# Optimization experiments

Measured on AMD Instinct MI355X. Metric: run time of the kernel, lower is better.

The kernel has to match this reference:

```python
import jax, jax.numpy as jnp
import numpy as np

EPS = 1e-5
D_MODEL, D_INNER, D_STATE, DT_RANK, K = 2048, 4096, 16, 128, 4

def setup_inputs() -> dict:
    key = jax.random.key(0)
    ks = jax.random.split(key, 13)
    B = 128
    s = lambda k, shape, sc=0.02: jax.random.normal(k, shape, jnp.float32) * sc
    return {
        "hidden_states": jax.random.normal(ks[0], (B, 1, D_MODEL), jnp.float32),
        "conv_state": jax.random.normal(ks[1], (B, D_INNER, K - 1), jnp.float32),
        "ssm_state": jax.random.normal(ks[2], (B, D_INNER, D_STATE), jnp.float32),
        "norm_w": jnp.ones((D_MODEL,), jnp.float32),
        "in_proj_w": s(ks[3], (2 * D_INNER, D_MODEL)),           # no bias (HF Mamba default)
        "conv_w": s(ks[4], (D_INNER, K), 0.1),                    # depthwise conv kernel
        "conv_b": s(ks[5], (D_INNER,), 0.1),
        "x_proj_w": s(ks[6], (DT_RANK + 2 * D_STATE, D_INNER)),
        "dt_proj_w": s(ks[7], (D_INNER, DT_RANK)),
        "dt_proj_b": s(ks[8], (D_INNER,), 0.1),
        "A_log": jnp.log(jnp.broadcast_to(jnp.arange(1, D_STATE + 1, dtype=jnp.float32), (D_INNER, D_STATE))),
        "D": jnp.ones((D_INNER,), jnp.float32),
        "out_proj_w": s(ks[9], (D_MODEL, D_INNER)),               # no bias
    }

def reference(hidden_states, conv_state, ssm_state, norm_w, in_proj_w, conv_w, conv_b,
              x_proj_w, dt_proj_w, dt_proj_b, A_log, D, out_proj_w):
    x = hidden_states[:, 0, :]                                   # (B, d_model)
    # RMSNorm (pre-norm)
    normed = x * jax.lax.rsqrt(jnp.mean(x * x, axis=-1, keepdims=True) + EPS) * norm_w
    # in_proj -> gate z and conv branch xc
    xz = normed @ in_proj_w.T                                    # (B, 2*d_inner)
    xc, z = jnp.split(xz, 2, axis=-1)
    # depthwise causal conv, single-step with rolling cache
    conv_in = jnp.concatenate([conv_state, xc[:, :, None]], axis=-1)  # (B, d_inner, K)
    new_conv_state = conv_in[:, :, 1:]
    xact = jax.nn.silu(jnp.sum(conv_in * conv_w[None], axis=-1) + conv_b)  # (B, d_inner)
    # input-dependent SSM params
    proj = xact @ x_proj_w.T                                     # (B, dt_rank + 2*d_state)
    dt_raw = proj[:, :DT_RANK]
    Bmat = proj[:, DT_RANK:DT_RANK + D_STATE]                    # (B, d_state)
    Cmat = proj[:, DT_RANK + D_STATE:]                           # (B, d_state)
    dt = jax.nn.softplus(dt_raw @ dt_proj_w.T + dt_proj_b)       # (B, d_inner)
    A = -jnp.exp(A_log)                                          # (d_inner, d_state)
    dA = jnp.exp(dt[:, :, None] * A[None])                       # (B, d_inner, d_state)
    dB = dt[:, :, None] * Bmat[:, None, :]
    new_ssm_state = ssm_state * dA + dB * xact[:, :, None]
    y = jnp.sum(new_ssm_state * Cmat[:, None, :], axis=-1) + D * xact
    y = y * jax.nn.silu(z)
    out = y @ out_proj_w.T                                       # (B, d_model)
    output = out[:, None, :] + hidden_states                     # residual add
    return output, new_conv_state, new_ssm_state
```

## Files before the change

kernel.cpp:

```cpp
#include <hip/hip_runtime.h>

typedef __attribute__((ext_vector_type(8))) short bf16x8;
typedef __attribute__((ext_vector_type(4))) float f32x4;
typedef __attribute__((ext_vector_type(8))) unsigned short u16x8;
typedef __attribute__((ext_vector_type(4))) unsigned short u16x4;

#define DM 2048
#define DI 4096
#define BATCH 128

__device__ __forceinline__ unsigned short f2bf(float f) {
  union { float f; unsigned u; } v; v.f = f;
  unsigned r = v.u + 0x7FFFu + ((v.u >> 16) & 1u);
  return (unsigned short)(r >> 16);
}
__device__ __forceinline__ float bf2f(unsigned short u) {
  union { unsigned u; float f; } v; v.u = (unsigned)u << 16; return v.f;
}
__device__ __forceinline__ float sigm(float x) { return 1.f / (1.f + __expf(-x)); }

constexpr int BK = 64;
constexpr int LDT = BK + 8;

#define LDREGS(AR, ARF, BR, kb_) do {                                                     \
    int kb = (kb_);                                                                       \
    if constexpr (ABF) {                                                                  \
      _Pragma("unroll") for (int i = 0; i < 4; ++i) {                                     \
        int idx = tid + i * 256, r = idx >> 3, c = (idx & 7) * 8;                         \
        AR[i] = *(const u16x8*)&((const unsigned short*)Ag)[(long)r * lda + kb + c];      \
      }                                                                                   \
    } else {                                                                              \
      _Pragma("unroll") for (int i = 0; i < 8; ++i) {                                     \
        int idx = tid + i * 256, r = idx >> 4, c = (idx & 15) * 4;                        \
        ARF[i] = *(const f32x4*)&((const float*)Ag)[(long)r * lda + kb + c];              \
      }                                                                                   \
    }                                                                                     \
    _Pragma("unroll") for (int i = 0; i < BN / 16; ++i) {                                 \
      int idx = tid + i * 256, r = idx >> 4, c = (idx & 15) * 4;                          \
      BR[i] = *(const f32x4*)&Bg[(long)(n0 + r) * ldb + kb + c];                          \
    }                                                                                     \
  } while (0)

#define STLDS(AR, ARF, BR, buf_) do {                                                     \
    unsigned short* As_ = lds + (buf_) * BUF;                                             \
    unsigned short* Bs_ = As_ + 128 * LDT;                                                \
    if constexpr (ABF) {                                                                  \
      _Pragma("unroll") for (int i = 0; i < 4; ++i) {                                     \
        int idx = tid + i * 256, r = idx >> 3, c = (idx & 7) * 8;                         \
        *(u16x8*)&As_[r * LDT + c] = AR[i];                                               \
      }                                                                                   \
    } else {                                                                              \
      _Pragma("unroll") for (int i = 0; i < 8; ++i) {                                     \
        int idx = tid + i * 256, r = idx >> 4, c = (idx & 15) * 4;                        \
        u16x4 o; o[0] = f2bf(ARF[i][0]); o[1] = f2bf(ARF[i][1]);                          \
        o[2] = f2bf(ARF[i][2]); o[3] = f2bf(ARF[i][3]);                                   \
        *(u16x4*)&As_[r * LDT + c] = o;                                                   \
      }                                                                                   \
    }                                                                                     \
    _Pragma("unroll") for (int i = 0; i < BN / 16; ++i) {                                 \
      int idx = tid + i * 256, r = idx >> 4, c = (idx & 15) * 4;                          \
      u16x4 o; o[0] = f2bf(BR[i][0]); o[1] = f2bf(BR[i][1]);                              \
      o[2] = f2bf(BR[i][2]); o[3] = f2bf(BR[i][3]);                                       \
      *(u16x4*)&Bs_[r * LDT + c] = o;                                                     \
    }                                                                                     \
  } while (0)

#define COMPUTE(buf_) do {                                                                \
    const unsigned short* As_ = lds + (buf_) * BUF;                                       \
    const unsigned short* Bs_ = As_ + 128 * LDT;                                          \
    _Pragma("unroll") for (int kk = 0; kk < BK; kk += 32) {                               \
      int kr = kk + lhi * 8;                                                              \
      bf16x8 af[4], bfr[NF];                                                              \
      _Pragma("unroll") for (int mi = 0; mi < 4; ++mi)                                    \
        af[mi] = *(const bf16x8*)&As_[(wm * 64 + mi * 16 + llo) * LDT + kr];              \
      _Pragma("unroll") for (int ni = 0; ni < NF; ++ni)                                   \
        bfr[ni] = *(const bf16x8*)&Bs_[(wn * 16 * NF + ni * 16 + llo) * LDT + kr];        \
      _Pragma("unroll") for (int mi = 0; mi < 4; ++mi)                                    \
        _Pragma("unroll") for (int ni = 0; ni < NF; ++ni)                                 \
          acc[mi * NF + ni] = __builtin_amdgcn_mfma_f32_16x16x32_bf16(                    \
              af[mi], bfr[ni], acc[mi * NF + ni], 0, 0, 0);                               \
    }                                                                                     \
  } while (0)

template<int BN, bool ABF>
__device__ __forceinline__ void gemm128(const void* Ag, int lda, const float* Bg, int ldb,
                                        int n0, int k0, int k1, unsigned short* lds,
                                        f32x4* acc) {
  constexpr int NF = BN / 32;
  constexpr int BUF = (128 + BN) * LDT;
  const int tid = threadIdx.x, lane = tid & 63, wave = tid >> 6;
  const int wm = wave >> 1, wn = wave & 1, llo = lane & 15, lhi = lane >> 4;

  u16x8 ar0[ABF ? 4 : 1], ar1[ABF ? 4 : 1];
  f32x4 arf0[ABF ? 1 : 8], arf1[ABF ? 1 : 8];
  f32x4 br0[BN / 16], br1[BN / 16];

  const int nt = (k1 - k0) / BK;
  LDREGS(ar0, arf0, br0, k0);
  LDREGS(ar1, arf1, br1, k0 + BK);
  STLDS(ar0, arf0, br0, 0);
  __syncthreads();
  int t = 0;
  while (true) {
    if (t + 2 < nt) LDREGS(ar0, arf0, br0, k0 + (t + 2) * BK);
    COMPUTE(0);
    if (t + 1 < nt) STLDS(ar1, arf1, br1, 1);
    __syncthreads();
    if (++t == nt) break;
    if (t + 2 < nt) LDREGS(ar1, arf1, br1, k0 + (t + 2) * BK);
    COMPUTE(1);
    if (t + 1 < nt) STLDS(ar0, arf0, br0, 0);
    __syncthreads();
    if (++t == nt) break;
  }
}

__global__ __launch_bounds__(256) void k01_prep(const float* __restrict__ hs,
                                                const float* __restrict__ nw,
                                                unsigned short* __restrict__ normed,
                                                float* __restrict__ outp,
                                                float* __restrict__ xz,
                                                float* __restrict__ proj) {
  int blk = blockIdx.x, tid = threadIdx.x;
  int t = blk * 256 + tid;
  f32x4 z = {};
  *(f32x4*)&xz[t * 4] = z;
  if (t < 65536) *(f32x4*)&outp[t * 4] = *(const f32x4*)&hs[t * 4];
  if (t < 5120) *(f32x4*)&proj[t * 4] = z;
  if (blk < 128) {
    int b = blk;
    const float* xr = hs + (long)b * DM;
    f32x4 v0 = *(const f32x4*)&xr[tid * 4];
    f32x4 v1 = *(const f32x4*)&xr[(tid + 256) * 4];
    float ss = v0[0]*v0[0] + v0[1]*v0[1] + v0[2]*v0[2] + v0[3]*v0[3]
             + v1[0]*v1[0] + v1[1]*v1[1] + v1[2]*v1[2] + v1[3]*v1[3];
    for (int off = 32; off; off >>= 1) ss += __shfl_xor(ss, off);
    __shared__ float red[4];
    if ((tid & 63) == 0) red[tid >> 6] = ss;
    __syncthreads();
    ss = red[0] + red[1] + red[2] + red[3];
    float rstd = rsqrtf(ss * (1.f / DM) + 1e-5f);
    f32x4 w0 = *(const f32x4*)&nw[tid * 4];
    f32x4 w1 = *(const f32x4*)&nw[(tid + 256) * 4];
    u16x4 o0, o1;
#pragma unroll
    for (int j = 0; j < 4; ++j) {
      o0[j] = f2bf(v0[j] * rstd * w0[j]);
      o1[j] = f2bf(v1[j] * rstd * w1[j]);
    }
    *(u16x4*)&normed[(long)b * DM + tid * 4] = o0;
    *(u16x4*)&normed[(long)b * DM + (tid + 256) * 4] = o1;
  }
}

__global__ __launch_bounds__(256) void k2_inproj(const unsigned short* __restrict__ normed,
                                                 const float* __restrict__ W,
                                                 float* __restrict__ xz) {
  __shared__ unsigned short lds[2 * (128 + 64) * LDT];
  f32x4 acc[8] = {};
  int bn = blockIdx.x, sk = blockIdx.y;
  gemm128<64, true>(normed, DM, W, DM, bn * 64, sk * 512, sk * 512 + 512, lds, acc);
  int tid = threadIdx.x, lane = tid & 63, wave = tid >> 6, wm = wave >> 1, wn = wave & 1;
  int llo = lane & 15, lhi = lane >> 4;
#pragma unroll
  for (int mi = 0; mi < 4; ++mi)
#pragma unroll
    for (int ni = 0; ni < 2; ++ni)
#pragma unroll
      for (int r = 0; r < 4; ++r) {
        int b = wm * 64 + mi * 16 + lhi * 4 + r;
        int n = bn * 64 + wn * 32 + ni * 16 + llo;
        atomicAdd(&xz[(long)b * 8192 + n], acc[mi * 2 + ni][r]);
      }
}

__global__ __launch_bounds__(256) void e2_conv(const float* __restrict__ xz,
                                               const float* __restrict__ conv_state,
                                               const float* __restrict__ conv_w,
                                               const float* __restrict__ conv_b,
                                               float* __restrict__ out_ncs,
                                               float* __restrict__ xact_f,
                                               unsigned short* __restrict__ xact_b,
                                               unsigned short* __restrict__ szb) {
  int p = blockIdx.x * 256 + threadIdx.x;
  int b = p >> 12, n = p & 4095;
  float xc = xz[(long)b * 8192 + n];
  float z  = xz[(long)b * 8192 + DI + n];
  const float* cs = conv_state + (long)p * 3;
  float c0 = cs[0], c1 = cs[1], c2 = cs[2];
  f32x4 cw = *(const f32x4*)&conv_w[n * 4];
  float xs = c0 * cw[0] + c1 * cw[1] + c2 * cw[2] + xc * cw[3] + conv_b[n];
  float xa = xs * sigm(xs);
  float* ncs = out_ncs + (long)p * 3;
  ncs[0] = c1; ncs[1] = c2; ncs[2] = xc;
  xact_f[p] = xa;
  xact_b[p] = f2bf(xa);
  szb[p] = f2bf(z * sigm(z));
}

__global__ __launch_bounds__(256) void k3_xproj(const unsigned short* __restrict__ xact_b,
                                                const float* __restrict__ XW,
                                                float* __restrict__ proj) {
  __shared__ unsigned short lds[2 * (128 + 32) * LDT];
  f32x4 acc[4] = {};
  int bn = blockIdx.x, kc = blockIdx.y;
  gemm128<32, true>(xact_b, DI, XW, DI, bn * 32, kc * 128, kc * 128 + 128, lds, acc);
  int tid = threadIdx.x, lane = tid & 63, wave = tid >> 6, wm = wave >> 1, wn = wave & 1;
  int llo = lane & 15, lhi = lane >> 4;
  int n = bn * 32 + wn * 16 + llo;
#pragma unroll
  for (int mi = 0; mi < 4; ++mi)
#pragma unroll
    for (int r = 0; r < 4; ++r) {
      int b = wm * 64 + mi * 16 + lhi * 4 + r;
      atomicAdd(&proj[b * 160 + n], acc[mi][r]);
    }
}

__global__ __launch_bounds__(256) void k4a_dt(const float* __restrict__ proj,
                                              const float* __restrict__ DW,
                                              const float* __restrict__ dtb,
                                              float* __restrict__ dt_f) {
  __shared__ unsigned short lds[2 * (128 + 32) * LDT];
  f32x4 acc[4] = {};
  int bn = blockIdx.x;
  gemm128<32, false>(proj, 160, DW, 128, bn * 32, 0, 128, lds, acc);
  int tid = threadIdx.x, lane = tid & 63, wave = tid >> 6, wm = wave >> 1, wn = wave & 1;
  int llo = lane & 15, lhi = lane >> 4;
  int n = bn * 32 + wn * 16 + llo;
  float db = dtb[n];
#pragma unroll
  for (int mi = 0; mi < 4; ++mi)
#pragma unroll
    for (int r = 0; r < 4; ++r) {
      int b = wm * 64 + mi * 16 + lhi * 4 + r;
      float v = acc[mi][r] + db;
      dt_f[(long)b * DI + n] = (v > 20.f) ? v : log1pf(__expf(v));
    }
}

__global__ __launch_bounds__(256) void k4b_ssm(const float* __restrict__ dt_f,
                                               const float* __restrict__ proj,
                                               const float* __restrict__ A_log,
                                               const float* __restrict__ Dp,
                                               const float* __restrict__ ssm,
                                               const float* __restrict__ xact_f,
                                               const unsigned short* __restrict__ szb,
                                               float* __restrict__ out_nss,
                                               unsigned short* __restrict__ yz_b) {
  int t = blockIdx.x * 256 + threadIdx.x;
  int s4 = t & 3;
  int p0 = t >> 2;
  const int STRIDE = (2048 * 256) >> 2;
#pragma unroll
  for (int it = 0; it < 4; ++it) {
    int p = p0 + it * STRIDE;
    int b = p >> 12, n = p & 4095;
    float dtv = dt_f[p];
    float xa = xact_f[p];
    f32x4 sv = *(const f32x4*)&ssm[(long)p * 16 + s4 * 4];
    f32x4 Al = *(const f32x4*)&A_log[n * 16 + s4 * 4];
    f32x4 Bv = *(const f32x4*)&proj[b * 160 + 128 + s4 * 4];
    f32x4 Cv = *(const f32x4*)&proj[b * 160 + 144 + s4 * 4];
    f32x4 nv;
    float y = 0.f;
#pragma unroll
    for (int j = 0; j < 4; ++j) {
      float dA = __expf(dtv * (-__expf(Al[j])));
      nv[j] = sv[j] * dA + dtv * Bv[j] * xa;
      y += nv[j] * Cv[j];
    }
    *(f32x4*)&out_nss[(long)p * 16 + s4 * 4] = nv;
    y += __shfl_xor(y, 1);
    y += __shfl_xor(y, 2);
    if (s4 == 0) yz_b[p] = f2bf((y + Dp[n] * xa) * bf2f(szb[p]));
  }
}

__global__ __launch_bounds__(256) void k5_outproj(const unsigned short* __restrict__ yz_b,
                                                  const float* __restrict__ OW,
                                                  float* __restrict__ outp) {
  __shared__ unsigned short lds[2 * (128 + 32) * LDT];
  f32x4 acc[4] = {};
  int bn = blockIdx.x, sk = blockIdx.y;
  gemm128<32, true>(yz_b, DI, OW, DI, bn * 32, sk * 512, sk * 512 + 512, lds, acc);
  int tid = threadIdx.x, lane = tid & 63, wave = tid >> 6, wm = wave >> 1, wn = wave & 1;
  int llo = lane & 15, lhi = lane >> 4;
  int n = bn * 32 + wn * 16 + llo;
#pragma unroll
  for (int mi = 0; mi < 4; ++mi)
#pragma unroll
    for (int r = 0; r < 4; ++r) {
      int b = wm * 64 + mi * 16 + lhi * 4 + r;
      atomicAdd(&outp[(long)b * DM + n], acc[mi][r]);
    }
}

extern "C" void kernel_launch(void* const* d_in, const int* in_sizes, int n_in, void* d_out,
                              int out_size, void* d_ws, size_t ws_size, hipStream_t stream) {
  const float* hs         = (const float*)d_in[0];
  const float* conv_state = (const float*)d_in[1];
  const float* ssm        = (const float*)d_in[2];
  const float* norm_w     = (const float*)d_in[3];
  const float* in_proj_w  = (const float*)d_in[4];
  const float* conv_w     = (const float*)d_in[5];
  const float* conv_b     = (const float*)d_in[6];
  const float* x_proj_w   = (const float*)d_in[7];
  const float* dt_proj_w  = (const float*)d_in[8];
  const float* dt_proj_b  = (const float*)d_in[9];
  const float* A_log      = (const float*)d_in[10];
  const float* Dp         = (const float*)d_in[11];
  const float* out_proj_w = (const float*)d_in[12];

  float* outp    = (float*)d_out;
  float* out_ncs = outp + 262144;
  float* out_nss = outp + 262144 + 1572864;

  char* ws = (char*)d_ws;
  unsigned short* normed = (unsigned short*)(ws);
  float*          dt_f   = (float*)(ws);
  float*          xz     = (float*)(ws + 2097152);
  unsigned short* yz_b   = (unsigned short*)(ws + 2097152);
  float*          xact_f = (float*)(ws + 6291456);
  unsigned short* xact_b = (unsigned short*)(ws + 8388608);
  unsigned short* szb    = (unsigned short*)(ws + 9437184);
  float*          proj   = (float*)(ws + 10485760);

  hipLaunchKernelGGL(k01_prep, dim3(1024), dim3(256), 0, stream, hs, norm_w, normed, outp, xz, proj);
  hipLaunchKernelGGL(k2_inproj, dim3(128, 4), dim3(256), 0, stream, normed, in_proj_w, xz);
  hipLaunchKernelGGL(e2_conv, dim3(2048), dim3(256), 0, stream, xz, conv_state, conv_w, conv_b,
                     out_ncs, xact_f, xact_b, szb);
  hipLaunchKernelGGL(k3_xproj, dim3(5, 32), dim3(256), 0, stream, xact_b, x_proj_w, proj);
  hipLaunchKernelGGL(k4a_dt, dim3(128), dim3(256), 0, stream, proj, dt_proj_w, dt_proj_b, dt_f);
  hipLaunchKernelGGL(k4b_ssm, dim3(2048), dim3(256), 0, stream, dt_f, proj, A_log, Dp, ssm,
                     xact_f, szb, out_nss, yz_b);
  hipLaunchKernelGGL(k5_outproj, dim3(64, 8), dim3(256), 0, stream, yz_b, out_proj_w, outp);
}
```

Measured before the change: 76.76 us.

## Fuse dt projection GEMM with SSM update and shrink in_proj N tile

Generalizes the GEMM helper to take an M tile size and offset. It then fuses the dt_proj GEMM and softplus into the selective-scan update kernel, so the dt intermediate is never written to or read from global memory and one launch disappears. The fused kernel uses 32x32 tiles over a 128x4 grid, and each thread handles all 16 states of a row with per-thread strided 64-byte loads. The in_proj kernel also switches from a 64-wide to a 32-wide N tile, doubling its block count for better occupancy. That costs more reloading of the A operand.

```diff
diff --git a/kernel.cpp b/kernel.cpp
--- a/kernel.cpp
+++ b/kernel.cpp
@@ -25,14 +25,14 @@
 #define LDREGS(AR, ARF, BR, kb_) do {                                                     \
     int kb = (kb_);                                                                       \
     if constexpr (ABF) {                                                                  \
-      _Pragma("unroll") for (int i = 0; i < 4; ++i) {                                     \
+      _Pragma("unroll") for (int i = 0; i < BM / 32; ++i) {                               \
         int idx = tid + i * 256, r = idx >> 3, c = (idx & 7) * 8;                         \
-        AR[i] = *(const u16x8*)&((const unsigned short*)Ag)[(long)r * lda + kb + c];      \
+        AR[i] = *(const u16x8*)&((const unsigned short*)Ag)[(long)(m0 + r) * lda + kb + c]; \
       }                                                                                   \
     } else {                                                                              \
-      _Pragma("unroll") for (int i = 0; i < 8; ++i) {                                     \
+      _Pragma("unroll") for (int i = 0; i < BM / 16; ++i) {                               \
         int idx = tid + i * 256, r = idx >> 4, c = (idx & 15) * 4;                        \
-        ARF[i] = *(const f32x4*)&((const float*)Ag)[(long)r * lda + kb + c];              \
+        ARF[i] = *(const f32x4*)&((const float*)Ag)[(long)(m0 + r) * lda + kb + c];       \
       }                                                                                   \
     }                                                                                     \
     _Pragma("unroll") for (int i = 0; i < BN / 16; ++i) {                                 \
@@ -43,14 +43,14 @@
 
 #define STLDS(AR, ARF, BR, buf_) do {                                                     \
     unsigned short* As_ = lds + (buf_) * BUF;                                             \
-    unsigned short* Bs_ = As_ + 128 * LDT;                                                \
+    unsigned short* Bs_ = As_ + BM * LDT;                                                 \
     if constexpr (ABF) {                                                                  \
-      _Pragma("unroll") for (int i = 0; i < 4; ++i) {                                     \
+      _Pragma("unroll") for (int i = 0; i < BM / 32; ++i) {                               \
         int idx = tid + i * 256, r = idx >> 3, c = (idx & 7) * 8;                         \
         *(u16x8*)&As_[r * LDT + c] = AR[i];                                               \
       }                                                                                   \
     } else {                                                                              \
-      _Pragma("unroll") for (int i = 0; i < 8; ++i) {                                     \
+      _Pragma("unroll") for (int i = 0; i < BM / 16; ++i) {                               \
         int idx = tid + i * 256, r = idx >> 4, c = (idx & 15) * 4;                        \
         u16x4 o; o[0] = f2bf(ARF[i][0]); o[1] = f2bf(ARF[i][1]);                          \
         o[2] = f2bf(ARF[i][2]); o[3] = f2bf(ARF[i][3]);                                   \
@@ -67,32 +67,33 @@
 
 #define COMPUTE(buf_) do {                                                                \
     const unsigned short* As_ = lds + (buf_) * BUF;                                       \
-    const unsigned short* Bs_ = As_ + 128 * LDT;                                          \
+    const unsigned short* Bs_ = As_ + BM * LDT;                                           \
     _Pragma("unroll") for (int kk = 0; kk < BK; kk += 32) {                               \
       int kr = kk + lhi * 8;                                                              \
-      bf16x8 af[4], bfr[NF];                                                              \
-      _Pragma("unroll") for (int mi = 0; mi < 4; ++mi)                                    \
-        af[mi] = *(const bf16x8*)&As_[(wm * 64 + mi * 16 + llo) * LDT + kr];              \
+      bf16x8 af[MI], bfr[NF];                                                             \
+      _Pragma("unroll") for (int mi = 0; mi < MI; ++mi)                                   \
+        af[mi] = *(const bf16x8*)&As_[(wm * (BM / 2) + mi * 16 + llo) * LDT + kr];        \
       _Pragma("unroll") for (int ni = 0; ni < NF; ++ni)                                   \
         bfr[ni] = *(const bf16x8*)&Bs_[(wn * 16 * NF + ni * 16 + llo) * LDT + kr];        \
-      _Pragma("unroll") for (int mi = 0; mi < 4; ++mi)                                    \
+      _Pragma("unroll") for (int mi = 0; mi < MI; ++mi)                                   \
         _Pragma("unroll") for (int ni = 0; ni < NF; ++ni)                                 \
           acc[mi * NF + ni] = __builtin_amdgcn_mfma_f32_16x16x32_bf16(                    \
               af[mi], bfr[ni], acc[mi * NF + ni], 0, 0, 0);                               \
     }                                                                                     \
   } while (0)
 
-template<int BN, bool ABF>
-__device__ __forceinline__ void gemm128(const void* Ag, int lda, const float* Bg, int ldb,
-                                        int n0, int k0, int k1, unsigned short* lds,
-                                        f32x4* acc) {
+template<int BM, int BN, bool ABF>
+__device__ __forceinline__ void gemmMN(const void* Ag, int lda, const float* Bg, int ldb,
+                                       int m0, int n0, int k0, int k1, unsigned short* lds,
+                                       f32x4* acc) {
   constexpr int NF = BN / 32;
-  constexpr int BUF = (128 + BN) * LDT;
+  constexpr int MI = BM / 32;
+  constexpr int BUF = (BM + BN) * LDT;
   const int tid = threadIdx.x, lane = tid & 63, wave = tid >> 6;
   const int wm = wave >> 1, wn = wave & 1, llo = lane & 15, lhi = lane >> 4;
 
-  u16x8 ar0[ABF ? 4 : 1], ar1[ABF ? 4 : 1];
-  f32x4 arf0[ABF ? 1 : 8], arf1[ABF ? 1 : 8];
+  u16x8 ar0[ABF ? BM / 32 : 1], ar1[ABF ? BM / 32 : 1];
+  f32x4 arf0[ABF ? 1 : BM / 16], arf1[ABF ? 1 : BM / 16];
   f32x4 br0[BN / 16], br1[BN / 16];
 
   const int nt = (k1 - k0) / BK;
@@ -156,22 +157,20 @@
 __global__ __launch_bounds__(256) void k2_inproj(const unsigned short* __restrict__ normed,
                                                  const float* __restrict__ W,
                                                  float* __restrict__ xz) {
-  __shared__ unsigned short lds[2 * (128 + 64) * LDT];
-  f32x4 acc[8] = {};
+  __shared__ unsigned short lds[2 * (128 + 32) * LDT];
+  f32x4 acc[4] = {};
   int bn = blockIdx.x, sk = blockIdx.y;
-  gemm128<64, true>(normed, DM, W, DM, bn * 64, sk * 512, sk * 512 + 512, lds, acc);
+  gemmMN<128, 32, true>(normed, DM, W, DM, 0, bn * 32, sk * 512, sk * 512 + 512, lds, acc);
   int tid = threadIdx.x, lane = tid & 63, wave = tid >> 6, wm = wave >> 1, wn = wave & 1;
   int llo = lane & 15, lhi = lane >> 4;
+  int n = bn * 32 + wn * 16 + llo;
 #pragma unroll
   for (int mi = 0; mi < 4; ++mi)
 #pragma unroll
-    for (int ni = 0; ni < 2; ++ni)
-#pragma unroll
-      for (int r = 0; r < 4; ++r) {
-        int b = wm * 64 + mi * 16 + lhi * 4 + r;
-        int n = bn * 64 + wn * 32 + ni * 16 + llo;
-        atomicAdd(&xz[(long)b * 8192 + n], acc[mi * 2 + ni][r]);
-      }
+    for (int r = 0; r < 4; ++r) {
+      int b = wm * 64 + mi * 16 + lhi * 4 + r;
+      atomicAdd(&xz[(long)b * 8192 + n], acc[mi][r]);
+    }
 }
 
 __global__ __launch_bounds__(256) void e2_conv(const float* __restrict__ xz,
@@ -204,7 +203,7 @@
   __shared__ unsigned short lds[2 * (128 + 32) * LDT];
   f32x4 acc[4] = {};
   int bn = blockIdx.x, kc = blockIdx.y;
-  gemm128<32, true>(xact_b, DI, XW, DI, bn * 32, kc * 128, kc * 128 + 128, lds, acc);
+  gemmMN<128, 32, true>(xact_b, DI, XW, DI, 0, bn * 32, kc * 128, kc * 128 + 128, lds, acc);
   int tid = threadIdx.x, lane = tid & 63, wave = tid >> 6, wm = wave >> 1, wn = wave & 1;
   int llo = lane & 15, lhi = lane >> 4;
   int n = bn * 32 + wn * 16 + llo;
@@ -217,63 +216,61 @@
     }
 }
 
-__global__ __launch_bounds__(256) void k4a_dt(const float* __restrict__ proj,
-                                              const float* __restrict__ DW,
-                                              const float* __restrict__ dtb,
-                                              float* __restrict__ dt_f) {
-  __shared__ unsigned short lds[2 * (128 + 32) * LDT];
-  f32x4 acc[4] = {};
-  int bn = blockIdx.x;
-  gemm128<32, false>(proj, 160, DW, 128, bn * 32, 0, 128, lds, acc);
+__global__ __launch_bounds__(256) void k45_dtssm(const float* __restrict__ proj,
+                                                 const float* __restrict__ DW,
+                                                 const float* __restrict__ dtb,
+                                                 const float* __restrict__ A_log,
+                                                 const float* __restrict__ Dp,
+                                                 const float* __restrict__ ssm,
+                                                 const float* __restrict__ xact_f,
+                                                 const unsigned short* __restrict__ szb,
+                                                 float* __restrict__ out_nss,
+                                                 unsigned short* __restrict__ yz_b) {
+  __shared__ unsigned short lds[2 * (32 + 32) * LDT];
+  f32x4 acc[1] = {};
+  int nb = blockIdx.x, mb = blockIdx.y;
+  gemmMN<32, 32, false>(proj, 160, DW, 128, mb * 32, nb * 32, 0, 128, lds, acc);
   int tid = threadIdx.x, lane = tid & 63, wave = tid >> 6, wm = wave >> 1, wn = wave & 1;
   int llo = lane & 15, lhi = lane >> 4;
-  int n = bn * 32 + wn * 16 + llo;
-  float db = dtb[n];
-#pragma unroll
-  for (int mi = 0; mi < 4; ++mi)
-#pragma unroll
-    for (int r = 0; r < 4; ++r) {
-      int b = wm * 64 + mi * 16 + lhi * 4 + r;
-      float v = acc[mi][r] + db;
-      dt_f[(long)b * DI + n] = (v > 20.f) ? v : log1pf(__expf(v));
-    }
-}
-
-__global__ __launch_bounds__(256) void k4b_ssm(const float* __restrict__ dt_f,
-                                               const float* __restrict__ proj,
-                                               const float* __restrict__ A_log,
-                                               const float* __restrict__ Dp,
-                                               const float* __restrict__ ssm,
-                                               const float* __restrict__ xact_f,
-                                               const unsigned short* __restrict__ szb,
-                                               float* __restrict__ out_nss,
-                                               unsigned short* __restrict__ yz_b) {
-  int t = blockIdx.x * 256 + threadIdx.x;
-  int s4 = t & 3;
-  int p0 = t >> 2;
-  const int STRIDE = (2048 * 256) >> 2;
-#pragma unroll
-  for (int it = 0; it < 4; ++it) {
-    int p = p0 + it * STRIDE;
-    int b = p >> 12, n = p & 4095;
-    float dtv = dt_f[p];
+  int n = nb * 32 + wn * 16 + llo;
+  float dtbn = dtb[n], Dn = Dp[n];
+  f32x4 Al0 = *(const f32x4*)&A_log[n * 16];
+  f32x4 Al1 = *(const f32x4*)&A_log[n * 16 + 4];
+  f32x4 Al2 = *(const f32x4*)&A_log[n * 16 + 8];
+  f32x4 Al3 = *(const f32x4*)&A_log[n * 16 + 12];
+  float aS[16];
+#pragma unroll
+  for (int j = 0; j < 4; ++j) {
+    aS[j] = -__expf(Al0[j]); aS[4 + j] = -__expf(Al1[j]);
+    aS[8 + j] = -__expf(Al2[j]); aS[12 + j] = -__expf(Al3[j]);
+  }
+#pragma unroll
+  for (int r = 0; r < 4; ++r) {
+    int b = mb * 32 + wm * 16 + lhi * 4 + r;
+    long p = (long)b * DI + n;
+    float v = acc[0][r] + dtbn;
+    float dtv = (v > 20.f) ? v : log1pf(__expf(v));
     float xa = xact_f[p];
-    f32x4 sv = *(const f32x4*)&ssm[(long)p * 16 + s4 * 4];
-    f32x4 Al = *(const f32x4*)&A_log[n * 16 + s4 * 4];
-    f32x4 Bv = *(const f32x4*)&proj[b * 160 + 128 + s4 * 4];
-    f32x4 Cv = *(const f32x4*)&proj[b * 160 + 144 + s4 * 4];
-    f32x4 nv;
+    const float* Bp = proj + b * 160 + 128;
+    const float* Cp = proj + b * 160 + 144;
+    const float* sp = ssm + p * 16;
+    float* np = out_nss + p * 16;
     float y = 0.f;
 #pragma unroll
-    for (int j = 0; j < 4; ++j) {
-      float dA = __expf(dtv * (-__expf(Al[j])));
-      nv[j] = sv[j] * dA + dtv * Bv[j] * xa;
-      y += nv[j] * Cv[j];
-    }
-    *(f32x4*)&out_nss[(long)p * 16 + s4 * 4] = nv;
-    y += __shfl_xor(y, 1);
-    y += __shfl_xor(y, 2);
-    if (s4 == 0) yz_b[p] = f2bf((y + Dp[n] * xa) * bf2f(szb[p]));
+    for (int q = 0; q < 4; ++q) {
+      f32x4 sv = *(const f32x4*)&sp[q * 4];
+      f32x4 Bv = *(const f32x4*)&Bp[q * 4];
+      f32x4 Cv = *(const f32x4*)&Cp[q * 4];
+      f32x4 nv;
+#pragma unroll
+      for (int j = 0; j < 4; ++j) {
+        float dA = __expf(dtv * aS[q * 4 + j]);
+        nv[j] = sv[j] * dA + dtv * Bv[j] * xa;
+        y += nv[j] * Cv[j];
+      }
+      *(f32x4*)&np[q * 4] = nv;
+    }
+    yz_b[p] = f2bf((y + Dn * xa) * bf2f(szb[p]));
   }
 }
 
@@ -283,7 +280,7 @@
   __shared__ unsigned short lds[2 * (128 + 32) * LDT];
   f32x4 acc[4] = {};
   int bn = blockIdx.x, sk = blockIdx.y;
-  gemm128<32, true>(yz_b, DI, OW, DI, bn * 32, sk * 512, sk * 512 + 512, lds, acc);
+  gemmMN<128, 32, true>(yz_b, DI, OW, DI, 0, bn * 32, sk * 512, sk * 512 + 512, lds, acc);
   int tid = threadIdx.x, lane = tid & 63, wave = tid >> 6, wm = wave >> 1, wn = wave & 1;
   int llo = lane & 15, lhi = lane >> 4;
   int n = bn * 32 + wn * 16 + llo;
@@ -318,7 +315,6 @@
 
   char* ws = (char*)d_ws;
   unsigned short* normed = (unsigned short*)(ws);
-  float*          dt_f   = (float*)(ws);
   float*          xz     = (float*)(ws + 2097152);
   unsigned short* yz_b   = (unsigned short*)(ws + 2097152);
   float*          xact_f = (float*)(ws + 6291456);
@@ -327,12 +323,11 @@
   float*          proj   = (float*)(ws + 10485760);
 
   hipLaunchKernelGGL(k01_prep, dim3(1024), dim3(256), 0, stream, hs, norm_w, normed, outp, xz, proj);
-  hipLaunchKernelGGL(k2_inproj, dim3(128, 4), dim3(256), 0, stream, normed, in_proj_w, xz);
+  hipLaunchKernelGGL(k2_inproj, dim3(256, 4), dim3(256), 0, stream, normed, in_proj_w, xz);
   hipLaunchKernelGGL(e2_conv, dim3(2048), dim3(256), 0, stream, xz, conv_state, conv_w, conv_b,
                      out_ncs, xact_f, xact_b, szb);
   hipLaunchKernelGGL(k3_xproj, dim3(5, 32), dim3(256), 0, stream, xact_b, x_proj_w, proj);
-  hipLaunchKernelGGL(k4a_dt, dim3(128), dim3(256), 0, stream, proj, dt_proj_w, dt_proj_b, dt_f);
-  hipLaunchKernelGGL(k4b_ssm, dim3(2048), dim3(256), 0, stream, dt_f, proj, A_log, Dp, ssm,
-                     xact_f, szb, out_nss, yz_b);
+  hipLaunchKernelGGL(k45_dtssm, dim3(128, 4), dim3(256), 0, stream, proj, dt_proj_w, dt_proj_b,
+                     A_log, Dp, ssm, xact_f, szb, out_nss, yz_b);
   hipLaunchKernelGGL(k5_outproj, dim3(64, 8), dim3(256), 0, stream, yz_b, out_proj_w, outp);
 }
```

Result: slower. 79.43 us (+3.5%).
